# Kernel optimization log

Measured on AMD Instinct MI355X. Metric: run time of the kernel, lower is better.

Reference implementation:

```python
import jax, jax.numpy as jnp
import numpy as np

H = 1024          # internal hidden (hidden_size_arg + 8)
L = 64            # max_length
S = 64            # encoder seq len
V = 32000         # vocab
EMB = H + L       # embedding dim
GIN = 2 * H + L   # gru input dim


def setup_inputs() -> dict:
    key = jax.random.key(0)
    ks = jax.random.split(key, 16)
    inp = {
        "word_input": jax.random.randint(ks[0], (1,), 0, V),
        "prev_context": jax.random.normal(ks[1], (1, 1, H), jnp.float32),
        "prev_hidden": jax.random.normal(ks[2], (1, 1, H), jnp.float32),
        "encoder_outputs": jax.random.normal(ks[3], (S, 1, H), jnp.float32),
        "sources": jax.random.randint(ks[4], (S, 1), 0, V),
        "targets": jax.random.randint(ks[5], (16, 1), 0, V),
        "ti": 0,
        "use_teacher_forcing": 1,
        # learned parameters
        "emb_table": jax.random.normal(ks[6], (V, EMB), jnp.float32) * 0.02,
        "gru_Wih": jax.random.normal(ks[7], (3 * H, GIN), jnp.float32) * 0.02,
        "gru_Whh": jax.random.normal(ks[8], (3 * H, H), jnp.float32) * 0.02,
        "gru_bih": jnp.zeros((3 * H,), jnp.float32),
        "gru_bhh": jnp.zeros((3 * H,), jnp.float32),
        "copy_W": jax.random.normal(ks[9], (H, H), jnp.float32) * 0.02,
        "copy_b": jnp.zeros((H,), jnp.float32),
        "gen_W": jax.random.normal(ks[10], (V, 2 * H), jnp.float32) * 0.02,
        "gen_b": jnp.zeros((V,), jnp.float32),
    }
    return inp


def reference(word_input, prev_context, prev_hidden, encoder_outputs, sources,
              targets, ti, use_teacher_forcing, emb_table, gru_Wih, gru_Whh,
              gru_bih, gru_bhh, copy_W, copy_b, gen_W, gen_b):
    # embedding lookup, [1,1,EMB] (dropout is identity at inference)
    embedded = emb_table[word_input[0]]
    # pointer locations: where current target word appears in source
    di = targets[ti, 0] if use_teacher_forcing else word_input[0]
    loc = (sources[:, 0] == di).astype(embedded.dtype)            # [S]
    loc = loc / jnp.maximum(jnp.sqrt(jnp.sum(loc * loc)), 1e-12)  # F.normalize p=2
    embedded = embedded.at[:S].set(loc)
    # GRU cell (single step, batch 1)
    x = jnp.concatenate([embedded, prev_context[0, 0]])           # [GIN]
    h = prev_hidden[0, 0]                                         # [H]
    gi = gru_Wih @ x + gru_bih
    gh = gru_Whh @ h + gru_bhh
    r = jax.nn.sigmoid(gi[:H] + gh[:H])
    z = jax.nn.sigmoid(gi[H:2 * H] + gh[H:2 * H])
    n = jnp.tanh(gi[2 * H:] + r * gh[2 * H:])
    h_new = (1.0 - z) * n + z * h                                 # [H]
    current_hidden = h_new.reshape(1, 1, H)
    enc = encoder_outputs[:, 0, :]                                # [S,H]
    # dot attention
    attn_weights = jax.nn.softmax(enc @ h_new).reshape(1, 1, S)
    attn_context = (attn_weights[0] @ enc).reshape(1, 1, H)
    # generate score over vocab
    joined = jnp.concatenate([h_new, attn_context[0, 0]])         # [2H]
    score_g = gen_W @ joined + gen_b                              # [V]
    # copy score (uses prev_hidden per original code)
    c_part = jnp.tanh(enc @ copy_W.T + copy_b)                    # [S,H]
    score_c = c_part @ prev_hidden[0, 0]                          # [S]
    probs = jax.nn.log_softmax(jnp.concatenate([score_g, score_c]))
    prob_g, prob_c = probs[:V], probs[V:]
    # carrier = prob_c @ one_hot(sources) without materializing [S,V]
    carrier = jnp.zeros((V,), probs.dtype).at[sources[:, 0]].add(prob_c)
    output = (prob_g + carrier).reshape(1, V)
    return output, attn_context, current_hidden, attn_weights
```

## Files before the change

kernel.cpp:

```cpp
#include <hip/hip_runtime.h>

#define H   1024
#define S   64
#define V   32000
#define EMB 1088
#define GIN 2112

#define WS_GI   2112
#define WS_GH   5184
#define WS_JOIN 8256
#define WS_SG   10304
#define WS_SC   42304
#define WS_LOGZ 42368
#define WS_FLAG 42369
#define WS_SCP  42376

typedef unsigned short ushort_t;
typedef unsigned int   uint_t;

__device__ __forceinline__ float b2f(ushort_t u) {
  union { uint_t i; float f; } v; v.i = ((uint_t)u) << 16; return v.f;
}
__device__ __forceinline__ float bl(uint_t u) {
  union { uint_t i; float f; } v; v.i = u << 16; return v.f;
}
__device__ __forceinline__ float bh(uint_t u) {
  union { uint_t i; float f; } v; v.i = u & 0xffff0000u; return v.f;
}
__device__ __forceinline__ ushort_t f2b(float f) {
  union { float f; uint_t u; } v; v.f = f;
  uint_t u = v.u;
  u += 0x7fffu + ((u >> 16) & 1u);
  return (ushort_t)(u >> 16);
}

struct L8 { float v[8]; };

template<bool B>
__device__ __forceinline__ L8 load8(const void* base, size_t idx) {
  L8 r;
  if (B) {
    uint4 pk = *(const uint4*)((const ushort_t*)base + idx);
    r.v[0]=bl(pk.x); r.v[1]=bh(pk.x); r.v[2]=bl(pk.y); r.v[3]=bh(pk.y);
    r.v[4]=bl(pk.z); r.v[5]=bh(pk.z); r.v[6]=bl(pk.w); r.v[7]=bh(pk.w);
  } else {
    const float4* p = (const float4*)((const float*)base + idx);
    float4 a = p[0], b = p[1];
    r.v[0]=a.x; r.v[1]=a.y; r.v[2]=a.z; r.v[3]=a.w;
    r.v[4]=b.x; r.v[5]=b.y; r.v[6]=b.z; r.v[7]=b.w;
  }
  return r;
}
template<bool B>
__device__ __forceinline__ float ld1(const void* base, size_t idx) {
  return B ? b2f(((const ushort_t*)base)[idx]) : ((const float*)base)[idx];
}
template<bool B>
__device__ __forceinline__ void st1(void* base, size_t idx, float f) {
  if (B) ((ushort_t*)base)[idx] = f2b(f);
  else   ((float*)base)[idx] = f;
}
__device__ __forceinline__ float dot8f(L8 w, const float* xp) {
  const float4* p = (const float4*)xp;
  float4 a = p[0], b = p[1];
  return w.v[0]*a.x + w.v[1]*a.y + w.v[2]*a.z + w.v[3]*a.w
       + w.v[4]*b.x + w.v[5]*b.y + w.v[6]*b.z + w.v[7]*b.w;
}
__device__ __forceinline__ int ws_flag(const float* ws) {
  return *(const int*)(ws + WS_FLAG);
}

template<bool B>
__device__ void gru_part(const void* Wih, const void* Whh, const void* bih,
                         const void* bhh, const void* ph, const void* emb_table,
                         const void* prev_context, const int* word_input,
                         const int* sources, int di, float* ws,
                         float* s_x, float* s_h, float* s_loc) {
  int tid = threadIdx.x;
  if (tid < 64) {
    bool m = (sources[tid] == di);
    unsigned long long bal = __ballot(m);
    int c = __popcll(bal);
    float inv = (c > 0) ? (1.0f / sqrtf((float)c)) : 0.0f;
    s_loc[tid] = m ? inv : 0.0f;
  }
  __syncthreads();
  int w = word_input[0];
  size_t eoff = (size_t)w * EMB;
  for (int i = tid; i < GIN; i += 256) {
    float v;
    if (i < S)        v = s_loc[i];
    else if (i < EMB) v = ld1<B>(emb_table, eoff + i);
    else              v = ld1<B>(prev_context, i - EMB);
    s_x[i] = v;
  }
  for (int i = tid; i < H; i += 256) s_h[i] = ld1<B>(ph, i);
  __syncthreads();
  int wave = tid >> 6, lane = tid & 63;
  int r = blockIdx.x * 4 + wave;
  size_t ro = (size_t)r * GIN;
  float sum1 = 0.f;
#pragma unroll
  for (int it = 0; it < 4; ++it) {
    int j = it * 512 + lane * 8;
    sum1 += dot8f(load8<B>(Wih, ro + j), s_x + j);
  }
  sum1 += ld1<B>(Wih, ro + 2048 + lane) * s_x[2048 + lane];
  size_t ho = (size_t)r * H;
  float sum2 = 0.f;
#pragma unroll
  for (int it = 0; it < 2; ++it) {
    int j = it * 512 + lane * 8;
    sum2 += dot8f(load8<B>(Whh, ho + j), s_h + j);
  }
#pragma unroll
  for (int off = 32; off; off >>= 1) {
    sum1 += __shfl_down(sum1, off);
    sum2 += __shfl_down(sum2, off);
  }
  if (lane == 0) {
    ws[WS_GI + r] = sum1 + ld1<B>(bih, r);
    ws[WS_GH + r] = sum2 + ld1<B>(bhh, r);
  }
}

template<bool B>
__device__ void copy_part(const void* enc, const void* copy_W,
                          const void* copy_b, const void* ph, float* ws,
                          float* s_part) {
  int tid = threadIdx.x, wave = tid >> 6, lane = tid & 63;
  int b = blockIdx.x - 768;
  int sg = b >> 5;
  int s0 = sg * 8;
  int g  = b & 31;
  int hh0 = (g * 4 + wave) * 8;
  if (tid < 8) s_part[tid] = 0.f;
  __syncthreads();

  float acc[64];
#pragma unroll
  for (int k = 0; k < 64; ++k) acc[k] = 0.f;

#pragma unroll
  for (int it = 0; it < 2; ++it) {
    int j = it * 512 + lane * 8;
    L8 e[8];
#pragma unroll
    for (int si = 0; si < 8; ++si)
      e[si] = load8<B>(enc, (size_t)(s0 + si) * H + j);
#pragma unroll
    for (int hi = 0; hi < 8; ++hi) {
      L8 w = load8<B>(copy_W, (size_t)(hh0 + hi) * H + j);
#pragma unroll
      for (int si = 0; si < 8; ++si) {
        float t = 0.f;
#pragma unroll
        for (int q = 0; q < 8; ++q) t += w.v[q] * e[si].v[q];
        acc[si * 8 + hi] += t;
      }
    }
  }
#pragma unroll
  for (int st = 5; st >= 0; --st) {
    int n = 1 << st;
    bool hi = (lane & n) != 0;
#pragma unroll
    for (int i = 0; i < 32; ++i) {
      if (i < n) {
        float keep = hi ? acc[i + n] : acc[i];
        float send = hi ? acc[i] : acc[i + n];
        acc[i] = keep + __shfl_xor(send, n);
      }
    }
  }
  int hi_idx = lane & 7;
  int si = lane >> 3;
  int hh = hh0 + hi_idx;
  float val = tanhf(acc[0] + ld1<B>(copy_b, hh)) * ld1<B>(ph, hh);
  val += __shfl_xor(val, 1);
  val += __shfl_xor(val, 2);
  val += __shfl_xor(val, 4);
  if (hi_idx == 0) atomicAdd(&s_part[si], val);
  __syncthreads();
  if (tid < 8)
    ws[WS_SCP + (size_t)(s0 + tid) * 32 + g] = s_part[tid];
}

__launch_bounds__(256)
__global__ void k_main(const int* word_input, const void* prev_context,
                       const void* ph, const void* enc, const int* sources,
                       const int* targets, const int* ti, const int* utf,
                       const void* emb_table, const void* Wih, const void* Whh,
                       const void* bih, const void* bhh, const void* copy_W,
                       const void* copy_b, const void* gen_W, float* ws) {
  __shared__ float s_x[GIN];
  __shared__ float s_h[H];
  __shared__ float s_loc[S];
  __shared__ float s_part[8];
  __shared__ int s_flag, s_di;
  int tid = threadIdx.x;
  if (tid < 64) {
    const ushort_t* g = (const ushort_t*)gen_W;
    int cnt = 0;
#pragma unroll
    for (int k = 0; k < 4; ++k) {
      float a = fabsf(b2f(g[2 * (tid + 64 * k)]));
      if (a >= 1e-5f && a <= 1.0f) ++cnt;
    }
#pragma unroll
    for (int off = 32; off; off >>= 1) cnt += __shfl_down(cnt, off);
    if (tid == 0) s_flag = (cnt >= 128) ? 1 : 0;
  }
  if (tid == 65) s_di = utf[0] ? targets[ti[0]] : word_input[0];
  __syncthreads();
  int FB = s_flag;
  if (blockIdx.x == 0 && tid == 0) *(int*)(ws + WS_FLAG) = FB;
  if (blockIdx.x < 768) {
    if (FB) gru_part<true >(Wih, Whh, bih, bhh, ph, emb_table, prev_context,
                            word_input, sources, s_di, ws, s_x, s_h, s_loc);
    else    gru_part<false>(Wih, Whh, bih, bhh, ph, emb_table, prev_context,
                            word_input, sources, s_di, ws, s_x, s_h, s_loc);
  } else {
    if (FB) copy_part<true >(enc, copy_W, copy_b, ph, ws, s_part);
    else    copy_part<false>(enc, copy_W, copy_b, ph, ws, s_part);
  }
}

template<bool B>
__device__ void mid_body(const void* ph, const void* enc, float* ws,
                         void* d_out, float* s_hn, float* s_sc, float* s_w) {
  int tid = threadIdx.x;
  {
    float gr = ws[WS_GI + tid]       + ws[WS_GH + tid];
    float gz = ws[WS_GI + H + tid]   + ws[WS_GH + H + tid];
    float r  = 1.f / (1.f + expf(-gr));
    float z  = 1.f / (1.f + expf(-gz));
    float n  = tanhf(ws[WS_GI + 2*H + tid] + r * ws[WS_GH + 2*H + tid]);
    float h  = ld1<B>(ph, tid);
    float hn = (1.f - z) * n + z * h;
    s_hn[tid] = hn;
    ws[WS_JOIN + tid] = hn;
    st1<B>(d_out, V + H + tid, hn);
  }
  __syncthreads();
  int wave = tid >> 6, lane = tid & 63;
#pragma unroll
  for (int q = 0; q < 4; ++q) {
    int s = wave + 16 * q;
    size_t eo = (size_t)s * H;
    float sum = 0.f;
#pragma unroll
    for (int it = 0; it < 2; ++it) {
      int j = it * 512 + lane * 8;
      sum += dot8f(load8<B>(enc, eo + j), s_hn + j);
    }
#pragma unroll
    for (int off = 32; off; off >>= 1) sum += __shfl_down(sum, off);
    if (lane == 0) s_sc[s] = sum;
  }
  __syncthreads();
  if (tid < 64) {
    float v = s_sc[tid];
    float m = v;
#pragma unroll
    for (int off = 32; off; off >>= 1) m = fmaxf(m, __shfl_xor(m, off));
    float e = expf(v - m);
    float sm = e;
#pragma unroll
    for (int off = 32; off; off >>= 1) sm += __shfl_xor(sm, off);
    float w = e / sm;
    s_w[tid] = w;
    st1<B>(d_out, V + 2*H + tid, w);
  }
  __syncthreads();
  float acc = 0.f;
#pragma unroll 4
  for (int s = 0; s < S; ++s) acc += s_w[s] * ld1<B>(enc, (size_t)s * H + tid);
  ws[WS_JOIN + H + tid] = acc;
  st1<B>(d_out, V + tid, acc);
}
__launch_bounds__(1024)
__global__ void k_mid(const void* ph, const void* enc, float* ws, void* d_out) {
  __shared__ float s_hn[H];
  __shared__ float s_sc[S];
  __shared__ float s_w[S];
  if (ws_flag(ws)) mid_body<true >(ph, enc, ws, d_out, s_hn, s_sc, s_w);
  else             mid_body<false>(ph, enc, ws, d_out, s_hn, s_sc, s_w);
}

template<bool B>
__device__ void gen_body(const void* gen_W, const void* gen_b, float* ws,
                         float* s_j) {
  int tid = threadIdx.x;
  for (int i = tid; i < 2 * H; i += 256) s_j[i] = ws[WS_JOIN + i];
  __syncthreads();
  int wave = tid >> 6, lane = tid & 63;
  int v0 = blockIdx.x * 8 + wave * 2;
#pragma unroll
  for (int rr = 0; rr < 2; ++rr) {
    int v = v0 + rr;
    size_t ro = (size_t)v * (2 * H);
    float sum = 0.f;
#pragma unroll
    for (int it = 0; it < 4; ++it) {
      int j = it * 512 + lane * 8;
      sum += dot8f(load8<B>(gen_W, ro + j), s_j + j);
    }
#pragma unroll
    for (int off = 32; off; off >>= 1) sum += __shfl_down(sum, off);
    if (lane == 0) ws[WS_SG + v] = sum + ld1<B>(gen_b, v);
  }
}
__launch_bounds__(256)
__global__ void k_gen(const void* gen_W, const void* gen_b, float* ws) {
  __shared__ float s_j[2 * H];
  if (ws_flag(ws)) gen_body<true >(gen_W, gen_b, ws, s_j);
  else             gen_body<false>(gen_W, gen_b, ws, s_j);
}

__launch_bounds__(1024)
__global__ void k_lse(float* ws) {
  __shared__ float red[16];
  __shared__ float s_M;
  __shared__ float s_sc[S];
  int tid = threadIdx.x;
  if (tid < 64) {
    float sc = 0.f;
#pragma unroll
    for (int g = 0; g < 32; ++g) sc += ws[WS_SCP + (size_t)tid * 32 + g];
    s_sc[tid] = sc;
    ws[WS_SC + tid] = sc;
  }
  __syncthreads();
  const float4* sc4 = (const float4*)(ws + WS_SG);
  float m = -3.0e38f;
  for (int i = tid; i < 8000; i += 1024) {
    float4 v = sc4[i];
    m = fmaxf(m, fmaxf(fmaxf(v.x, v.y), fmaxf(v.z, v.w)));
  }
  if (tid < 64) m = fmaxf(m, s_sc[tid]);
#pragma unroll
  for (int off = 32; off; off >>= 1) m = fmaxf(m, __shfl_xor(m, off));
  int wave = tid >> 6;
  if ((tid & 63) == 0) red[wave] = m;
  __syncthreads();
  if (tid == 0) {
    float mm = red[0];
    for (int i = 1; i < 16; ++i) mm = fmaxf(mm, red[i]);
    s_M = mm;
  }
  __syncthreads();
  float M = s_M;
  float sum = 0.f;
  for (int i = tid; i < 8000; i += 1024) {
    float4 v = sc4[i];
    sum += expf(v.x - M) + expf(v.y - M) + expf(v.z - M) + expf(v.w - M);
  }
  if (tid < 64) sum += expf(s_sc[tid] - M);
#pragma unroll
  for (int off = 32; off; off >>= 1) sum += __shfl_xor(sum, off);
  if ((tid & 63) == 0) red[wave] = sum;
  __syncthreads();
  if (tid == 0) {
    float ss = 0.f;
    for (int i = 0; i < 16; ++i) ss += red[i];
    ws[WS_LOGZ] = M + logf(ss);
  }
}

template<bool B>
__device__ void final_body(const int* sources, const float* ws, void* d_out,
                           int* s_src, float* s_pc) {
  int tid = threadIdx.x;
  float logZ = ws[WS_LOGZ];
  if (tid < 64) {
    s_src[tid] = sources[tid];
    s_pc[tid] = ws[WS_SC + tid] - logZ;
  }
  __syncthreads();
  int v = blockIdx.x * 256 + tid;
  float acc = ws[WS_SG + v] - logZ;
#pragma unroll
  for (int i = 0; i < S; ++i) acc += (s_src[i] == v) ? s_pc[i] : 0.f;
  st1<B>(d_out, v, acc);
}
__global__ void k_final(const int* sources, const float* ws, void* d_out) {
  __shared__ int   s_src[S];
  __shared__ float s_pc[S];
  if (ws_flag(ws)) final_body<true >(sources, ws, d_out, s_src, s_pc);
  else             final_body<false>(sources, ws, d_out, s_src, s_pc);
}

extern "C" void kernel_launch(void* const* d_in, const int* in_sizes, int n_in,
                              void* d_out, int out_size, void* d_ws, size_t ws_size,
                              hipStream_t stream) {
  const int*  word_input   = (const int*)d_in[0];
  const void* prev_context = d_in[1];
  const void* prev_hidden  = d_in[2];
  const void* enc          = d_in[3];
  const int*  sources      = (const int*)d_in[4];
  const int*  targets      = (const int*)d_in[5];
  const int*  ti           = (const int*)d_in[6];
  const int*  utf          = (const int*)d_in[7];
  const void* emb_table    = d_in[8];
  const void* gru_Wih      = d_in[9];
  const void* gru_Whh      = d_in[10];
  const void* gru_bih      = d_in[11];
  const void* gru_bhh      = d_in[12];
  const void* copy_W       = d_in[13];
  const void* copy_b       = d_in[14];
  const void* gen_W        = d_in[15];
  const void* gen_b        = d_in[16];
  float* ws = (float*)d_ws;

  k_main <<<1024, 256, 0, stream>>>(word_input, prev_context, prev_hidden, enc,
                                    sources, targets, ti, utf, emb_table,
                                    gru_Wih, gru_Whh, gru_bih, gru_bhh,
                                    copy_W, copy_b, gen_W, ws);
  k_mid  <<<1,   1024, 0, stream>>>(prev_hidden, enc, ws, d_out);
  k_gen  <<<4000, 256, 0, stream>>>(gen_W, gen_b, ws);
  k_lse  <<<1,   1024, 0, stream>>>(ws);
  k_final<<<125,  256, 0, stream>>>(sources, ws, d_out);
}
```

Baseline: 488.9 us.

## Fuse all five kernels into one persistent kernel with grid barriers

Replaces the five-kernel launch sequence with a single 512-block persistent kernel that separates the GRU/copy, attention, generator GEMV and log-softmax phases with atomic grid-wide barriers. It also redistributes work: each wave handles three GRU rows and sixteen vocab rows, and every finalizing block recomputes the log-sum-exp redundantly instead of relying on a single-block reduction kernel. The aim is to remove kernel-launch gaps and the serialized single-block kernels. In exchange it depends on all 512 blocks being co-resident for the spin barriers, adds a memset launch to reset the counters, and runs the attention phase on one block of 256 threads instead of 1024.

```diff
diff --git a/kernel.cpp b/kernel.cpp
--- a/kernel.cpp
+++ b/kernel.cpp
@@ -11,9 +11,9 @@
 #define WS_JOIN 8256
 #define WS_SG   10304
 #define WS_SC   42304
-#define WS_LOGZ 42368
-#define WS_FLAG 42369
 #define WS_SCP  42376
+
+#define NBLK 512
 
 typedef unsigned short ushort_t;
 typedef unsigned int   uint_t;
@@ -66,138 +66,296 @@
   return w.v[0]*a.x + w.v[1]*a.y + w.v[2]*a.z + w.v[3]*a.w
        + w.v[4]*b.x + w.v[5]*b.y + w.v[6]*b.z + w.v[7]*b.w;
 }
-__device__ __forceinline__ int ws_flag(const float* ws) {
-  return *(const int*)(ws + WS_FLAG);
-}
+
+__device__ __forceinline__ void gridbar(int* c) {
+  __threadfence();
+  __syncthreads();
+  if (threadIdx.x == 0) {
+    __hip_atomic_fetch_add(c, 1, __ATOMIC_ACQ_REL, __HIP_MEMORY_SCOPE_AGENT);
+    int it = 0;
+    while (__hip_atomic_load(c, __ATOMIC_ACQUIRE, __HIP_MEMORY_SCOPE_AGENT)
+               < NBLK && it < 4000000) {
+      __builtin_amdgcn_s_sleep(2);
+      ++it;
+    }
+  }
+  __syncthreads();
+}
+
+struct Sm {
+  float s_x[GIN];
+  float s_h[H];
+  float s_loc[S];
+  float s_part[8];
+  float s_hn[H];
+  float s_sc[S];
+  float s_w[S];
+  float s_j[2 * H];
+  float red[4];
+  float s_pc[S];
+  int   s_src[S];
+  int   s_di;
+};
 
 template<bool B>
-__device__ void gru_part(const void* Wih, const void* Whh, const void* bih,
-                         const void* bhh, const void* ph, const void* emb_table,
-                         const void* prev_context, const int* word_input,
-                         const int* sources, int di, float* ws,
-                         float* s_x, float* s_h, float* s_loc) {
-  int tid = threadIdx.x;
-  if (tid < 64) {
-    bool m = (sources[tid] == di);
-    unsigned long long bal = __ballot(m);
-    int c = __popcll(bal);
-    float inv = (c > 0) ? (1.0f / sqrtf((float)c)) : 0.0f;
-    s_loc[tid] = m ? inv : 0.0f;
-  }
+__device__ void body(const int* word_input, const void* prev_context,
+                     const void* ph, const void* enc, const int* sources,
+                     const void* emb_table, const void* Wih, const void* Whh,
+                     const void* bih, const void* bhh, const void* copy_W,
+                     const void* copy_b, const void* gen_W, const void* gen_b,
+                     float* ws, void* d_out, Sm* sm, int di) {
+  int tid  = threadIdx.x;
+  int bid  = blockIdx.x;
+  int wave = tid >> 6, lane = tid & 63;
+  int* bar = (int*)ws;
+
+  if (bid < 256) {
+    if (tid < 64) {
+      bool m = (sources[tid] == di);
+      unsigned long long bal = __ballot(m);
+      int c = __popcll(bal);
+      float inv = (c > 0) ? (1.0f / sqrtf((float)c)) : 0.0f;
+      sm->s_loc[tid] = m ? inv : 0.0f;
+    }
+    __syncthreads();
+    int w = word_input[0];
+    size_t eoff = (size_t)w * EMB;
+    for (int i = tid; i < GIN; i += 256) {
+      float v;
+      if (i < S)        v = sm->s_loc[i];
+      else if (i < EMB) v = ld1<B>(emb_table, eoff + i);
+      else              v = ld1<B>(prev_context, i - EMB);
+      sm->s_x[i] = v;
+    }
+    for (int i = tid; i < H; i += 256) sm->s_h[i] = ld1<B>(ph, i);
+    __syncthreads();
+    int wg = bid * 4 + wave;
+#pragma unroll
+    for (int rr = 0; rr < 3; ++rr) {
+      int r = wg * 3 + rr;
+      size_t ro = (size_t)r * GIN;
+      float sum1 = 0.f;
+#pragma unroll
+      for (int it = 0; it < 4; ++it) {
+        int j = it * 512 + lane * 8;
+        sum1 += dot8f(load8<B>(Wih, ro + j), sm->s_x + j);
+      }
+      sum1 += ld1<B>(Wih, ro + 2048 + lane) * sm->s_x[2048 + lane];
+      size_t ho = (size_t)r * H;
+      float sum2 = 0.f;
+#pragma unroll
+      for (int it = 0; it < 2; ++it) {
+        int j = it * 512 + lane * 8;
+        sum2 += dot8f(load8<B>(Whh, ho + j), sm->s_h + j);
+      }
+#pragma unroll
+      for (int off = 32; off; off >>= 1) {
+        sum1 += __shfl_down(sum1, off);
+        sum2 += __shfl_down(sum2, off);
+      }
+      if (lane == 0) {
+        ws[WS_GI + r] = sum1 + ld1<B>(bih, r);
+        ws[WS_GH + r] = sum2 + ld1<B>(bhh, r);
+      }
+    }
+  } else {
+    int b  = bid - 256;
+    int sg = b >> 5;
+    int s0 = sg * 8;
+    int g  = b & 31;
+    int hh0 = (g * 4 + wave) * 8;
+    if (tid < 8) sm->s_part[tid] = 0.f;
+    __syncthreads();
+
+    float acc[64];
+#pragma unroll
+    for (int k = 0; k < 64; ++k) acc[k] = 0.f;
+#pragma unroll
+    for (int it = 0; it < 2; ++it) {
+      int j = it * 512 + lane * 8;
+      L8 e[8];
+#pragma unroll
+      for (int si = 0; si < 8; ++si)
+        e[si] = load8<B>(enc, (size_t)(s0 + si) * H + j);
+#pragma unroll
+      for (int hi = 0; hi < 8; ++hi) {
+        L8 wv = load8<B>(copy_W, (size_t)(hh0 + hi) * H + j);
+#pragma unroll
+        for (int si = 0; si < 8; ++si) {
+          float t = 0.f;
+#pragma unroll
+          for (int q = 0; q < 8; ++q) t += wv.v[q] * e[si].v[q];
+          acc[si * 8 + hi] += t;
+        }
+      }
+    }
+#pragma unroll
+    for (int st = 5; st >= 0; --st) {
+      int n = 1 << st;
+      bool hi = (lane & n) != 0;
+#pragma unroll
+      for (int i = 0; i < 32; ++i) {
+        if (i < n) {
+          float keep = hi ? acc[i + n] : acc[i];
+          float send = hi ? acc[i] : acc[i + n];
+          acc[i] = keep + __shfl_xor(send, n);
+        }
+      }
+    }
+    int hi_idx = lane & 7;
+    int si = lane >> 3;
+    int hh = hh0 + hi_idx;
+    float val = tanhf(acc[0] + ld1<B>(copy_b, hh)) * ld1<B>(ph, hh);
+    val += __shfl_xor(val, 1);
+    val += __shfl_xor(val, 2);
+    val += __shfl_xor(val, 4);
+    if (hi_idx == 0) atomicAdd(&sm->s_part[si], val);
+    __syncthreads();
+    if (tid < 8)
+      ws[WS_SCP + (size_t)(s0 + tid) * 32 + g] = sm->s_part[tid];
+  }
+  gridbar(bar + 0);
+
+  if (bid == 0) {
+    for (int i = tid; i < H; i += 256) {
+      float gr = ws[WS_GI + i]     + ws[WS_GH + i];
+      float gz = ws[WS_GI + H + i] + ws[WS_GH + H + i];
+      float r  = 1.f / (1.f + expf(-gr));
+      float z  = 1.f / (1.f + expf(-gz));
+      float n  = tanhf(ws[WS_GI + 2*H + i] + r * ws[WS_GH + 2*H + i]);
+      float h  = ld1<B>(ph, i);
+      sm->s_hn[i] = (1.f - z) * n + z * h;
+    }
+    __syncthreads();
+#pragma unroll 2
+    for (int q = 0; q < 16; ++q) {
+      int s = wave * 16 + q;
+      size_t eo = (size_t)s * H;
+      float sum = 0.f;
+#pragma unroll
+      for (int it = 0; it < 2; ++it) {
+        int j = it * 512 + lane * 8;
+        sum += dot8f(load8<B>(enc, eo + j), sm->s_hn + j);
+      }
+#pragma unroll
+      for (int off = 32; off; off >>= 1) sum += __shfl_down(sum, off);
+      if (lane == 0) sm->s_sc[s] = sum;
+    }
+    __syncthreads();
+    if (tid < 64) {
+      float vv = sm->s_sc[tid];
+      float m = vv;
+#pragma unroll
+      for (int off = 32; off; off >>= 1) m = fmaxf(m, __shfl_xor(m, off));
+      float e = expf(vv - m);
+      float smx = e;
+#pragma unroll
+      for (int off = 32; off; off >>= 1) smx += __shfl_xor(smx, off);
+      float wgt = e / smx;
+      sm->s_w[tid] = wgt;
+      st1<B>(d_out, V + 2*H + tid, wgt);
+    }
+    __syncthreads();
+    for (int i = tid; i < H; i += 256) {
+      float acc = 0.f;
+#pragma unroll 4
+      for (int s = 0; s < S; ++s)
+        acc += sm->s_w[s] * ld1<B>(enc, (size_t)s * H + i);
+      ws[WS_JOIN + H + i] = acc;
+      st1<B>(d_out, V + i, acc);
+    }
+  } else if (bid == 1) {
+    if (tid < 64) {
+      float sc = 0.f;
+#pragma unroll
+      for (int g2 = 0; g2 < 32; ++g2) sc += ws[WS_SCP + (size_t)tid * 32 + g2];
+      ws[WS_SC + tid] = sc;
+    }
+  } else if (bid < 6) {
+    int i = (bid - 2) * 256 + tid;
+    float gr = ws[WS_GI + i]     + ws[WS_GH + i];
+    float gz = ws[WS_GI + H + i] + ws[WS_GH + H + i];
+    float r  = 1.f / (1.f + expf(-gr));
+    float z  = 1.f / (1.f + expf(-gz));
+    float n  = tanhf(ws[WS_GI + 2*H + i] + r * ws[WS_GH + 2*H + i]);
+    float h  = ld1<B>(ph, i);
+    float hn = (1.f - z) * n + z * h;
+    ws[WS_JOIN + i] = hn;
+    st1<B>(d_out, V + H + i, hn);
+  }
+  gridbar(bar + 1);
+
+  for (int i = tid; i < 2 * H; i += 256) sm->s_j[i] = ws[WS_JOIN + i];
   __syncthreads();
-  int w = word_input[0];
-  size_t eoff = (size_t)w * EMB;
-  for (int i = tid; i < GIN; i += 256) {
-    float v;
-    if (i < S)        v = s_loc[i];
-    else if (i < EMB) v = ld1<B>(emb_table, eoff + i);
-    else              v = ld1<B>(prev_context, i - EMB);
-    s_x[i] = v;
-  }
-  for (int i = tid; i < H; i += 256) s_h[i] = ld1<B>(ph, i);
-  __syncthreads();
-  int wave = tid >> 6, lane = tid & 63;
-  int r = blockIdx.x * 4 + wave;
-  size_t ro = (size_t)r * GIN;
-  float sum1 = 0.f;
-#pragma unroll
-  for (int it = 0; it < 4; ++it) {
-    int j = it * 512 + lane * 8;
-    sum1 += dot8f(load8<B>(Wih, ro + j), s_x + j);
-  }
-  sum1 += ld1<B>(Wih, ro + 2048 + lane) * s_x[2048 + lane];
-  size_t ho = (size_t)r * H;
-  float sum2 = 0.f;
-#pragma unroll
-  for (int it = 0; it < 2; ++it) {
-    int j = it * 512 + lane * 8;
-    sum2 += dot8f(load8<B>(Whh, ho + j), s_h + j);
-  }
-#pragma unroll
-  for (int off = 32; off; off >>= 1) {
-    sum1 += __shfl_down(sum1, off);
-    sum2 += __shfl_down(sum2, off);
-  }
-  if (lane == 0) {
-    ws[WS_GI + r] = sum1 + ld1<B>(bih, r);
-    ws[WS_GH + r] = sum2 + ld1<B>(bhh, r);
-  }
-}
-
-template<bool B>
-__device__ void copy_part(const void* enc, const void* copy_W,
-                          const void* copy_b, const void* ph, float* ws,
-                          float* s_part) {
-  int tid = threadIdx.x, wave = tid >> 6, lane = tid & 63;
-  int b = blockIdx.x - 768;
-  int sg = b >> 5;
-  int s0 = sg * 8;
-  int g  = b & 31;
-  int hh0 = (g * 4 + wave) * 8;
-  if (tid < 8) s_part[tid] = 0.f;
-  __syncthreads();
-
-  float acc[64];
-#pragma unroll
-  for (int k = 0; k < 64; ++k) acc[k] = 0.f;
-
-#pragma unroll
-  for (int it = 0; it < 2; ++it) {
-    int j = it * 512 + lane * 8;
-    L8 e[8];
-#pragma unroll
-    for (int si = 0; si < 8; ++si)
-      e[si] = load8<B>(enc, (size_t)(s0 + si) * H + j);
-#pragma unroll
-    for (int hi = 0; hi < 8; ++hi) {
-      L8 w = load8<B>(copy_W, (size_t)(hh0 + hi) * H + j);
-#pragma unroll
-      for (int si = 0; si < 8; ++si) {
-        float t = 0.f;
-#pragma unroll
-        for (int q = 0; q < 8; ++q) t += w.v[q] * e[si].v[q];
-        acc[si * 8 + hi] += t;
-      }
-    }
-  }
-#pragma unroll
-  for (int st = 5; st >= 0; --st) {
-    int n = 1 << st;
-    bool hi = (lane & n) != 0;
-#pragma unroll
-    for (int i = 0; i < 32; ++i) {
-      if (i < n) {
-        float keep = hi ? acc[i + n] : acc[i];
-        float send = hi ? acc[i] : acc[i + n];
-        acc[i] = keep + __shfl_xor(send, n);
-      }
-    }
-  }
-  int hi_idx = lane & 7;
-  int si = lane >> 3;
-  int hh = hh0 + hi_idx;
-  float val = tanhf(acc[0] + ld1<B>(copy_b, hh)) * ld1<B>(ph, hh);
-  val += __shfl_xor(val, 1);
-  val += __shfl_xor(val, 2);
-  val += __shfl_xor(val, 4);
-  if (hi_idx == 0) atomicAdd(&s_part[si], val);
-  __syncthreads();
-  if (tid < 8)
-    ws[WS_SCP + (size_t)(s0 + tid) * 32 + g] = s_part[tid];
-}
-
-__launch_bounds__(256)
-__global__ void k_main(const int* word_input, const void* prev_context,
-                       const void* ph, const void* enc, const int* sources,
-                       const int* targets, const int* ti, const int* utf,
-                       const void* emb_table, const void* Wih, const void* Whh,
-                       const void* bih, const void* bhh, const void* copy_W,
-                       const void* copy_b, const void* gen_W, float* ws) {
-  __shared__ float s_x[GIN];
-  __shared__ float s_h[H];
-  __shared__ float s_loc[S];
-  __shared__ float s_part[8];
-  __shared__ int s_flag, s_di;
+  {
+    int gw = bid * 4 + wave;
+    int base = gw * 16;
+#pragma unroll 2
+    for (int q = 0; q < 16; ++q) {
+      int v = base + q;
+      if (v < V) {
+        size_t ro = (size_t)v * (2 * H);
+        float sum = 0.f;
+#pragma unroll
+        for (int it = 0; it < 4; ++it) {
+          int j = it * 512 + lane * 8;
+          sum += dot8f(load8<B>(gen_W, ro + j), sm->s_j + j);
+        }
+#pragma unroll
+        for (int off = 32; off; off >>= 1) sum += __shfl_down(sum, off);
+        if (lane == 0) ws[WS_SG + v] = sum + ld1<B>(gen_b, v);
+      }
+    }
+  }
+  gridbar(bar + 2);
+
+  if (bid < 125) {
+    const float4* sc4 = (const float4*)(ws + WS_SG);
+    float m = -3.0e38f;
+    for (int i = tid; i < 8016; i += 256) {
+      float4 v = sc4[i];
+      m = fmaxf(m, fmaxf(fmaxf(v.x, v.y), fmaxf(v.z, v.w)));
+    }
+#pragma unroll
+    for (int off = 32; off; off >>= 1) m = fmaxf(m, __shfl_xor(m, off));
+    if (lane == 0) sm->red[wave] = m;
+    __syncthreads();
+    float M = fmaxf(fmaxf(sm->red[0], sm->red[1]),
+                    fmaxf(sm->red[2], sm->red[3]));
+    __syncthreads();
+    float sum = 0.f;
+    for (int i = tid; i < 8016; i += 256) {
+      float4 v = sc4[i];
+      sum += expf(v.x - M) + expf(v.y - M) + expf(v.z - M) + expf(v.w - M);
+    }
+#pragma unroll
+    for (int off = 32; off; off >>= 1) sum += __shfl_xor(sum, off);
+    if (lane == 0) sm->red[wave] = sum;
+    __syncthreads();
+    float logZ = M + logf(sm->red[0] + sm->red[1] + sm->red[2] + sm->red[3]);
+    if (tid < 64) {
+      sm->s_src[tid] = sources[tid];
+      sm->s_pc[tid]  = ws[WS_SC + tid] - logZ;
+    }
+    __syncthreads();
+    int v = bid * 256 + tid;
+    float acc = ws[WS_SG + v] - logZ;
+#pragma unroll
+    for (int i = 0; i < S; ++i) acc += (sm->s_src[i] == v) ? sm->s_pc[i] : 0.f;
+    st1<B>(d_out, v, acc);
+  }
+}
+
+__launch_bounds__(256, 2)
+__global__ void k_all(const int* word_input, const void* prev_context,
+                      const void* ph, const void* enc, const int* sources,
+                      const int* targets, const int* ti, const int* utf,
+                      const void* emb_table, const void* Wih, const void* Whh,
+                      const void* bih, const void* bhh, const void* copy_W,
+                      const void* copy_b, const void* gen_W, const void* gen_b,
+                      float* ws, void* d_out) {
+  __shared__ Sm sm;
+  __shared__ int s_flag;
   int tid = threadIdx.x;
   if (tid < 64) {
     const ushort_t* g = (const ushort_t*)gen_W;
@@ -211,184 +369,16 @@
     for (int off = 32; off; off >>= 1) cnt += __shfl_down(cnt, off);
     if (tid == 0) s_flag = (cnt >= 128) ? 1 : 0;
   }
-  if (tid == 65) s_di = utf[0] ? targets[ti[0]] : word_input[0];
+  if (tid == 65) sm.s_di = utf[0] ? targets[ti[0]] : word_input[0];
   __syncthreads();
   int FB = s_flag;
-  if (blockIdx.x == 0 && tid == 0) *(int*)(ws + WS_FLAG) = FB;
-  if (blockIdx.x < 768) {
-    if (FB) gru_part<true >(Wih, Whh, bih, bhh, ph, emb_table, prev_context,
-                            word_input, sources, s_di, ws, s_x, s_h, s_loc);
-    else    gru_part<false>(Wih, Whh, bih, bhh, ph, emb_table, prev_context,
-                            word_input, sources, s_di, ws, s_x, s_h, s_loc);
-  } else {
-    if (FB) copy_part<true >(enc, copy_W, copy_b, ph, ws, s_part);
-    else    copy_part<false>(enc, copy_W, copy_b, ph, ws, s_part);
-  }
-}
-
-template<bool B>
-__device__ void mid_body(const void* ph, const void* enc, float* ws,
-                         void* d_out, float* s_hn, float* s_sc, float* s_w) {
-  int tid = threadIdx.x;
-  {
-    float gr = ws[WS_GI + tid]       + ws[WS_GH + tid];
-    float gz = ws[WS_GI + H + tid]   + ws[WS_GH + H + tid];
-    float r  = 1.f / (1.f + expf(-gr));
-    float z  = 1.f / (1.f + expf(-gz));
-    float n  = tanhf(ws[WS_GI + 2*H + tid] + r * ws[WS_GH + 2*H + tid]);
-    float h  = ld1<B>(ph, tid);
-    float hn = (1.f - z) * n + z * h;
-    s_hn[tid] = hn;
-    ws[WS_JOIN + tid] = hn;
-    st1<B>(d_out, V + H + tid, hn);
-  }
-  __syncthreads();
-  int wave = tid >> 6, lane = tid & 63;
-#pragma unroll
-  for (int q = 0; q < 4; ++q) {
-    int s = wave + 16 * q;
-    size_t eo = (size_t)s * H;
-    float sum = 0.f;
-#pragma unroll
-    for (int it = 0; it < 2; ++it) {
-      int j = it * 512 + lane * 8;
-      sum += dot8f(load8<B>(enc, eo + j), s_hn + j);
-    }
-#pragma unroll
-    for (int off = 32; off; off >>= 1) sum += __shfl_down(sum, off);
-    if (lane == 0) s_sc[s] = sum;
-  }
-  __syncthreads();
-  if (tid < 64) {
-    float v = s_sc[tid];
-    float m = v;
-#pragma unroll
-    for (int off = 32; off; off >>= 1) m = fmaxf(m, __shfl_xor(m, off));
-    float e = expf(v - m);
-    float sm = e;
-#pragma unroll
-    for (int off = 32; off; off >>= 1) sm += __shfl_xor(sm, off);
-    float w = e / sm;
-    s_w[tid] = w;
-    st1<B>(d_out, V + 2*H + tid, w);
-  }
-  __syncthreads();
-  float acc = 0.f;
-#pragma unroll 4
-  for (int s = 0; s < S; ++s) acc += s_w[s] * ld1<B>(enc, (size_t)s * H + tid);
-  ws[WS_JOIN + H + tid] = acc;
-  st1<B>(d_out, V + tid, acc);
-}
-__launch_bounds__(1024)
-__global__ void k_mid(const void* ph, const void* enc, float* ws, void* d_out) {
-  __shared__ float s_hn[H];
-  __shared__ float s_sc[S];
-  __shared__ float s_w[S];
-  if (ws_flag(ws)) mid_body<true >(ph, enc, ws, d_out, s_hn, s_sc, s_w);
-  else             mid_body<false>(ph, enc, ws, d_out, s_hn, s_sc, s_w);
-}
-
-template<bool B>
-__device__ void gen_body(const void* gen_W, const void* gen_b, float* ws,
-                         float* s_j) {
-  int tid = threadIdx.x;
-  for (int i = tid; i < 2 * H; i += 256) s_j[i] = ws[WS_JOIN + i];
-  __syncthreads();
-  int wave = tid >> 6, lane = tid & 63;
-  int v0 = blockIdx.x * 8 + wave * 2;
-#pragma unroll
-  for (int rr = 0; rr < 2; ++rr) {
-    int v = v0 + rr;
-    size_t ro = (size_t)v * (2 * H);
-    float sum = 0.f;
-#pragma unroll
-    for (int it = 0; it < 4; ++it) {
-      int j = it * 512 + lane * 8;
-      sum += dot8f(load8<B>(gen_W, ro + j), s_j + j);
-    }
-#pragma unroll
-    for (int off = 32; off; off >>= 1) sum += __shfl_down(sum, off);
-    if (lane == 0) ws[WS_SG + v] = sum + ld1<B>(gen_b, v);
-  }
-}
-__launch_bounds__(256)
-__global__ void k_gen(const void* gen_W, const void* gen_b, float* ws) {
-  __shared__ float s_j[2 * H];
-  if (ws_flag(ws)) gen_body<true >(gen_W, gen_b, ws, s_j);
-  else             gen_body<false>(gen_W, gen_b, ws, s_j);
-}
-
-__launch_bounds__(1024)
-__global__ void k_lse(float* ws) {
-  __shared__ float red[16];
-  __shared__ float s_M;
-  __shared__ float s_sc[S];
-  int tid = threadIdx.x;
-  if (tid < 64) {
-    float sc = 0.f;
-#pragma unroll
-    for (int g = 0; g < 32; ++g) sc += ws[WS_SCP + (size_t)tid * 32 + g];
-    s_sc[tid] = sc;
-    ws[WS_SC + tid] = sc;
-  }
-  __syncthreads();
-  const float4* sc4 = (const float4*)(ws + WS_SG);
-  float m = -3.0e38f;
-  for (int i = tid; i < 8000; i += 1024) {
-    float4 v = sc4[i];
-    m = fmaxf(m, fmaxf(fmaxf(v.x, v.y), fmaxf(v.z, v.w)));
-  }
-  if (tid < 64) m = fmaxf(m, s_sc[tid]);
-#pragma unroll
-  for (int off = 32; off; off >>= 1) m = fmaxf(m, __shfl_xor(m, off));
-  int wave = tid >> 6;
-  if ((tid & 63) == 0) red[wave] = m;
-  __syncthreads();
-  if (tid == 0) {
-    float mm = red[0];
-    for (int i = 1; i < 16; ++i) mm = fmaxf(mm, red[i]);
-    s_M = mm;
-  }
-  __syncthreads();
-  float M = s_M;
-  float sum = 0.f;
-  for (int i = tid; i < 8000; i += 1024) {
-    float4 v = sc4[i];
-    sum += expf(v.x - M) + expf(v.y - M) + expf(v.z - M) + expf(v.w - M);
-  }
-  if (tid < 64) sum += expf(s_sc[tid] - M);
-#pragma unroll
-  for (int off = 32; off; off >>= 1) sum += __shfl_xor(sum, off);
-  if ((tid & 63) == 0) red[wave] = sum;
-  __syncthreads();
-  if (tid == 0) {
-    float ss = 0.f;
-    for (int i = 0; i < 16; ++i) ss += red[i];
-    ws[WS_LOGZ] = M + logf(ss);
-  }
-}
-
-template<bool B>
-__device__ void final_body(const int* sources, const float* ws, void* d_out,
-                           int* s_src, float* s_pc) {
-  int tid = threadIdx.x;
-  float logZ = ws[WS_LOGZ];
-  if (tid < 64) {
-    s_src[tid] = sources[tid];
-    s_pc[tid] = ws[WS_SC + tid] - logZ;
-  }
-  __syncthreads();
-  int v = blockIdx.x * 256 + tid;
-  float acc = ws[WS_SG + v] - logZ;
-#pragma unroll
-  for (int i = 0; i < S; ++i) acc += (s_src[i] == v) ? s_pc[i] : 0.f;
-  st1<B>(d_out, v, acc);
-}
-__global__ void k_final(const int* sources, const float* ws, void* d_out) {
-  __shared__ int   s_src[S];
-  __shared__ float s_pc[S];
-  if (ws_flag(ws)) final_body<true >(sources, ws, d_out, s_src, s_pc);
-  else             final_body<false>(sources, ws, d_out, s_src, s_pc);
+  int di = sm.s_di;
+  if (FB) body<true >(word_input, prev_context, ph, enc, sources, emb_table,
+                      Wih, Whh, bih, bhh, copy_W, copy_b, gen_W, gen_b,
+                      ws, d_out, &sm, di);
+  else    body<false>(word_input, prev_context, ph, enc, sources, emb_table,
+                      Wih, Whh, bih, bhh, copy_W, copy_b, gen_W, gen_b,
+                      ws, d_out, &sm, di);
 }
 
 extern "C" void kernel_launch(void* const* d_in, const int* in_sizes, int n_in,
@@ -413,12 +403,10 @@
   const void* gen_b        = d_in[16];
   float* ws = (float*)d_ws;
 
-  k_main <<<1024, 256, 0, stream>>>(word_input, prev_context, prev_hidden, enc,
-                                    sources, targets, ti, utf, emb_table,
-                                    gru_Wih, gru_Whh, gru_bih, gru_bhh,
-                                    copy_W, copy_b, gen_W, ws);
-  k_mid  <<<1,   1024, 0, stream>>>(prev_hidden, enc, ws, d_out);
-  k_gen  <<<4000, 256, 0, stream>>>(gen_W, gen_b, ws);
-  k_lse  <<<1,   1024, 0, stream>>>(ws);
-  k_final<<<125,  256, 0, stream>>>(sources, ws, d_out);
-}
+  hipMemsetAsync(ws, 0, 64, stream);
+
+  k_all<<<NBLK, 256, 0, stream>>>(word_input, prev_context, prev_hidden, enc,
+                                  sources, targets, ti, utf, emb_table,
+                                  gru_Wih, gru_Whh, gru_bih, gru_bhh,
+                                  copy_W, copy_b, gen_W, gen_b, ws, d_out);
+}
```

Result: slower. 935.5 us (+91.4%).
